# Kernel tuning notes

Hardware: AMD Instinct MI355X
Metric: run time of the kernel (lower is better)

Reference implementation:

```python
import jax, jax.numpy as jnp
import numpy as np

N_NODES = 100_000
N_EDGES = 1_600_000
N_GRAPHS = 512
IN_C, HID_C, OUT_C = 17, 64, 32


def setup_inputs() -> dict:
    key = jax.random.key(0)
    ks = jax.random.split(key, 12)
    x = jax.random.normal(ks[0], (N_NODES, IN_C), dtype=jnp.float32)
    edge_index = jax.random.randint(ks[1], (2, N_EDGES), 0, N_NODES, dtype=jnp.int64)
    batch = jnp.sort(jax.random.randint(ks[2], (N_NODES,), 0, N_GRAPHS, dtype=jnp.int64))
    def lin(k, fan_in, fan_out):
        s = 1.0 / np.sqrt(fan_in)
        kw, kb = jax.random.split(k)
        W = jax.random.uniform(kw, (fan_in, fan_out), minval=-s, maxval=s, dtype=jnp.float32)
        b = jax.random.uniform(kb, (fan_out,), minval=-s, maxval=s, dtype=jnp.float32)
        return W, b
    W1, b1 = lin(ks[3], IN_C, HID_C)      # GCNConv 1
    W2, b2 = lin(ks[4], HID_C, OUT_C)     # GCNConv 2
    Wf1, bf1 = lin(ks[5], OUT_C, OUT_C)   # fc1
    Wf2, bf2 = lin(ks[6], OUT_C, OUT_C)   # fc2
    return {"x": x, "edge_index": edge_index, "batch": batch,
            "W1": W1, "b1": b1, "W2": W2, "b2": b2,
            "Wf1": Wf1, "bf1": bf1, "Wf2": Wf2, "bf2": bf2}


def _gcn_conv(x, src, dst, norm, W, b, n_nodes):
    # PyG GCNConv: h = x @ W; out_i = sum_{j->i} norm_ij * h_j; out += bias
    h = x @ W                                   # [N, d_out]
    msg = h[src] * norm[:, None]                # gather + scale [E+N, d_out]
    out = jax.ops.segment_sum(msg, dst, num_segments=n_nodes)
    return out + b


def reference(x, edge_index, batch, W1, b1, W2, b2, Wf1, bf1, Wf2, bf2):
    n = x.shape[0]
    loops = jnp.arange(n, dtype=edge_index.dtype)
    src = jnp.concatenate([edge_index[0], loops])  # add self loops
    dst = jnp.concatenate([edge_index[1], loops])
    # symmetric normalization: deg^-1/2[src] * deg^-1/2[dst]
    deg = jax.ops.segment_sum(jnp.ones_like(dst, dtype=x.dtype), dst, num_segments=n)
    dinv = jnp.where(deg > 0, 1.0 / jnp.sqrt(deg), 0.0)
    norm = dinv[src] * dinv[dst]

    h = jax.nn.relu(_gcn_conv(x, src, dst, norm, W1, b1, n))
    h = _gcn_conv(h, src, dst, norm, W2, b2, n)

    # global mean pool over graphs
    cnt = jax.ops.segment_sum(jnp.ones((n,), dtype=h.dtype), batch, num_segments=N_GRAPHS)
    pooled = jax.ops.segment_sum(h, batch, num_segments=N_GRAPHS) / jnp.clip(cnt, 1.0)[:, None]

    out = jax.nn.relu(pooled @ Wf1 + bf1)
    out = out @ Wf2 + bf2
    return out  # [N_GRAPHS, OUT_C]
```

## Files before the change

### kernel.cpp

```cpp
#include <hip/hip_runtime.h>

#define IN_C 17
#define HID  64
#define OUTC 32

#define CH   8192
#define TA   512
#define NBP  512
#define BCAP 5632
#define SCAP 1024
#define BS_BLKS 8

typedef __attribute__((ext_vector_type(2))) float f2;
typedef __attribute__((ext_vector_type(8))) short bf16x8;
typedef __attribute__((ext_vector_type(4))) float f32x4;
__device__ __forceinline__ f2 mkf2(float x, float y) { f2 r; r.x = x; r.y = y; return r; }

__device__ __forceinline__ unsigned short f2bf(float f) {
    unsigned u = __float_as_uint(f);
    u += 0x7fffu + ((u >> 16) & 1u);
    return (unsigned short)(u >> 16);
}
__device__ __forceinline__ float bflo(unsigned u) { return __uint_as_float(u << 16); }
__device__ __forceinline__ float bfhi(unsigned u) { return __uint_as_float(u & 0xffff0000u); }

__global__ __launch_bounds__(TA) void k_binA(const int* __restrict__ src,
        const int* __restrict__ dst, int E,
        int* __restrict__ outbuf, int* __restrict__ cntmat, int* __restrict__ offmat) {
    __shared__ int cnt[NBP];
    __shared__ int off[NBP];
    __shared__ int stage[CH];
    int t = threadIdx.x;
    long base = (long)blockIdx.x * CH;
    int nE = (int)(E - base); if (nE > CH) nE = CH;
    cnt[t] = 0;
    __syncthreads();
    int bk[16], pk[16], rk[16];
#pragma unroll
    for (int j = 0; j < 16; ++j) {
        int idx = t + j * TA;
        if (idx < nE) {
            long e = base + idx;
            int d = __builtin_nontemporal_load(&dst[e]);
            int s = __builtin_nontemporal_load(&src[e]);
            int b = d >> 8;
            bk[j] = b;
            pk[j] = s | ((d & 255) << 17);
            rk[j] = atomicAdd(&cnt[b], 1);
        } else bk[j] = -1;
    }
    __syncthreads();
    int c = cnt[t];
    off[t] = c;
    __syncthreads();
    int inc = c;
    for (int s = 1; s < NBP; s <<= 1) {
        int add = (t >= s) ? off[t - s] : 0;
        __syncthreads();
        inc += add; off[t] = inc;
        __syncthreads();
    }
    int excl = inc - c;
    __syncthreads();
    off[t] = excl;
    __syncthreads();
#pragma unroll
    for (int j = 0; j < 16; ++j)
        if (bk[j] >= 0) stage[off[bk[j]] + rk[j]] = pk[j];
    __syncthreads();
    for (int i = t; i < nE; i += TA) outbuf[base + i] = stage[i];
    cntmat[blockIdx.x * NBP + t] = c;
    offmat[blockIdx.x * NBP + t] = excl;
}

__global__ __launch_bounds__(NBP) void k_bsum1(const int* __restrict__ cntmat,
        int nblkA, int* __restrict__ part, float* __restrict__ pool, int poolN) {
    int t = threadIdx.x, b = blockIdx.x;
    int per = (nblkA + BS_BLKS - 1) / BS_BLKS;
    int i0 = b * per, i1 = min(i0 + per, nblkA);
    int s = 0;
    for (int i = i0; i < i1; ++i) s += cntmat[i * NBP + t];
    part[b * NBP + t] = s;
    for (int i = b * NBP + t; i < poolN; i += BS_BLKS * NBP) pool[i] = 0.f;
}

__global__ __launch_bounds__(NBP) void k_bsum2(const int* __restrict__ part,
        int* __restrict__ bbase, const float* __restrict__ W2,
        uint4* __restrict__ w2frag) {
    __shared__ int sh[NBP];
    int t = threadIdx.x;
    int s = 0;
#pragma unroll
    for (int i = 0; i < BS_BLKS; ++i) s += part[i * NBP + t];
    sh[t] = s;
    __syncthreads();
    int inc = s;
    for (int st = 1; st < NBP; st <<= 1) {
        int add = (t >= st) ? sh[t - st] : 0;
        __syncthreads();
        inc += add; sh[t] = inc;
        __syncthreads();
    }
    bbase[t] = inc - s;
    if (t < 256) {
        int f = t >> 6, l = t & 63;
        int kt = f >> 1, nt = f & 1;
        int kbase = kt * 32 + (l >> 4) * 8;
        int c = nt * 16 + (l & 15);
        unsigned short v[8];
#pragma unroll
        for (int j = 0; j < 8; ++j) v[j] = f2bf(W2[(kbase + j) * OUTC + c]);
        uint4 o;
        o.x = (unsigned)v[0] | ((unsigned)v[1] << 16);
        o.y = (unsigned)v[2] | ((unsigned)v[3] << 16);
        o.z = (unsigned)v[4] | ((unsigned)v[5] << 16);
        o.w = (unsigned)v[6] | ((unsigned)v[7] << 16);
        w2frag[f * 64 + l] = o;
    }
}

__global__ __launch_bounds__(TA) void k_binB(const int* __restrict__ outbuf,
        const int* __restrict__ cntmat, const int* __restrict__ offmat,
        const int* __restrict__ bbase, int nblkA, int N,
        int* __restrict__ csr, int2* __restrict__ meta,
        const float* __restrict__ x, unsigned* __restrict__ xs16h,
        unsigned short* __restrict__ xs17h) {
    __shared__ int segc[256], sego[256], segs[256];
    __shared__ int ndeg[256], noff[256];
    __shared__ int stage[BCAP];
    int t = threadIdx.x, b = blockIdx.x;
    if (t < 256) {
        int cc = 0, ss = 0;
        if (t < nblkA) { cc = cntmat[t * NBP + b]; ss = offmat[t * NBP + b]; }
        segc[t] = cc; segs[t] = ss; sego[t] = cc;
        ndeg[t] = 0;
    }
    __syncthreads();
    {
        int c = (t < 256) ? sego[t] : 0;
        int inc = c;
        for (int s = 1; s < 256; s <<= 1) {
            int add = (t < 256 && t >= s) ? sego[t - s] : 0;
            __syncthreads();
            if (t < 256) { inc += add; sego[t] = inc; }
            __syncthreads();
        }
        if (t < 256) sego[t] = inc - c;
    }
    __syncthreads();
    int wave = t >> 6, lane = t & 63;
    for (int i = wave; i < nblkA; i += TA / 64) {
        int c = segc[i], so = sego[i];
        long gs = (long)i * CH + segs[i];
        for (int l = lane; l < c; l += 64) {
            int p = so + l;
            if (p < BCAP) stage[p] = __builtin_nontemporal_load(&outbuf[gs + l]);
        }
    }
    __syncthreads();
    int T = sego[255] + segc[255];
    if (T > BCAP) T = BCAP;
    int mypk[11], myrk[11], ne = 0;
    for (int k = t; k < T; k += TA) {
        int p = stage[k];
        int l = (p >> 17) & 255;
        myrk[ne] = atomicAdd(&ndeg[l], 1);
        mypk[ne] = p;
        ne++;
    }
    __syncthreads();
    {
        int c = (t < 256) ? ndeg[t] : 0;
        if (t < 256) noff[t] = c;
        __syncthreads();
        int inc = c;
        for (int s = 1; s < 256; s <<= 1) {
            int add = (t < 256 && t >= s) ? noff[t - s] : 0;
            __syncthreads();
            if (t < 256) { inc += add; noff[t] = inc; }
            __syncthreads();
        }
        if (t < 256) noff[t] = inc - c;
    }
    __syncthreads();
    int gb = bbase[b];
    int n0 = b << 8;
    if (t < 256 && n0 + t < N) {
        int n = n0 + t;
        meta[n] = make_int2(gb + noff[t], ndeg[t]);
        float dinv = rsqrtf((float)(ndeg[t] + 1));
        const float* xr = x + (size_t)n * IN_C;
        unsigned* xo = xs16h + (size_t)n * 8;
#pragma unroll
        for (int w2 = 0; w2 < 8; ++w2) {
            unsigned lo = f2bf(xr[2 * w2] * dinv);
            unsigned hi = f2bf(xr[2 * w2 + 1] * dinv);
            xo[w2] = lo | (hi << 16);
        }
        xs17h[n] = f2bf(xr[16] * dinv);
    }
    for (int j = 0; j < ne; ++j) {
        int p = mypk[j];
        int l = (p >> 17) & 255;
        csr[gb + noff[l] + myrk[j]] = p & 0x1FFFF;
    }
}

__global__ __launch_bounds__(256) void k_gather1(
        const uint4* __restrict__ xs16v, const unsigned short* __restrict__ xs17h,
        const int* __restrict__ csr, const int2* __restrict__ meta,
        const float* __restrict__ W1, const float* __restrict__ b1,
        unsigned short* __restrict__ h1b, int N) {
    __shared__ __align__(16) float aggx[16][20];
    __shared__ float dinv_sh[16];
    __shared__ int csr_sh[SCAP];

    int tid = threadIdx.x;
    int n0 = blockIdx.x * 16;
    int nlast = min(n0 + 15, N - 1);
    int2 m0 = meta[n0];
    int2 mlv = meta[nlast];
    int s_lo = m0.x;
    int seglen = mlv.x + mlv.y - s_lo;
    int sg = min(seglen, SCAP);
    for (int i = tid; i < sg; i += 256)
        csr_sh[i] = __builtin_nontemporal_load(&csr[s_lo + i]);
    int ch = tid & 63;
    float w1r[IN_C];
#pragma unroll
    for (int k = 0; k < IN_C; ++k) w1r[k] = W1[k * HID + ch];
    float b1v = b1[ch];
    __syncthreads();

    int ln = tid >> 4, sl = tid & 15;
    int n = n0 + ln;
    f2 acc[8];
#pragma unroll
    for (int j = 0; j < 8; ++j) acc[j] = mkf2(0.f, 0.f);
    float a17 = 0.f;
    if (n < N) {
        int2 m = meta[n];
        int start = m.x, cnt = m.y, end = start + cnt;
        auto body = [&](int s) {
            uint4 v0 = xs16v[(size_t)s * 2];
            uint4 v1 = xs16v[(size_t)s * 2 + 1];
            acc[0] += mkf2(bflo(v0.x), bfhi(v0.x));
            acc[1] += mkf2(bflo(v0.y), bfhi(v0.y));
            acc[2] += mkf2(bflo(v0.z), bfhi(v0.z));
            acc[3] += mkf2(bflo(v0.w), bfhi(v0.w));
            acc[4] += mkf2(bflo(v1.x), bfhi(v1.x));
            acc[5] += mkf2(bflo(v1.y), bfhi(v1.y));
            acc[6] += mkf2(bflo(v1.z), bfhi(v1.z));
            acc[7] += mkf2(bflo(v1.w), bfhi(v1.w));
            a17 += bflo((unsigned)xs17h[s]);
        };
        if (seglen <= SCAP) {
            for (int k = start + sl; k < end; k += 16) body(csr_sh[k - s_lo]);
        } else {
            for (int k = start + sl; k < end; k += 16)
                body(__builtin_nontemporal_load(&csr[k]));
        }
        if (sl == 0) {
            body(n);
            dinv_sh[ln] = rsqrtf((float)(cnt + 1));
        }
    }
    float a[16];
#pragma unroll
    for (int j = 0; j < 8; ++j) { a[2 * j] = acc[j].x; a[2 * j + 1] = acc[j].y; }
#pragma unroll
    for (int j = 0; j < 8; ++j) {
        float tt = (sl & 8) ? a[j + 8] : a[j];
        float uu = (sl & 8) ? a[j] : a[j + 8];
        a[j] = tt + __shfl_xor(uu, 8);
    }
#pragma unroll
    for (int j = 0; j < 4; ++j) {
        float tt = (sl & 4) ? a[j + 4] : a[j];
        float uu = (sl & 4) ? a[j] : a[j + 4];
        a[j] = tt + __shfl_xor(uu, 4);
    }
#pragma unroll
    for (int j = 0; j < 2; ++j) {
        float tt = (sl & 2) ? a[j + 2] : a[j];
        float uu = (sl & 2) ? a[j] : a[j + 2];
        a[j] = tt + __shfl_xor(uu, 2);
    }
    {
        float tt = (sl & 1) ? a[1] : a[0];
        float uu = (sl & 1) ? a[0] : a[1];
        a[0] = tt + __shfl_xor(uu, 1);
    }
    a17 += __shfl_xor(a17, 1);
    a17 += __shfl_xor(a17, 2);
    a17 += __shfl_xor(a17, 4);
    a17 += __shfl_xor(a17, 8);
    aggx[ln][sl] = a[0];
    if (sl == 0) aggx[ln][16] = a17;
    __syncthreads();
    int s0 = tid >> 6;
#pragma unroll
    for (int rep = 0; rep < 4; ++rep) {
        int slot = s0 + rep * 4;
        int nn = n0 + slot;
        if (nn < N) {
            const float4* ap = (const float4*)aggx[slot];
            float4 A0 = ap[0], A1 = ap[1], A2 = ap[2], A3 = ap[3];
            float a16 = aggx[slot][16];
            float dot = A0.x * w1r[0]  + A0.y * w1r[1]  + A0.z * w1r[2]  + A0.w * w1r[3]
                      + A1.x * w1r[4]  + A1.y * w1r[5]  + A1.z * w1r[6]  + A1.w * w1r[7]
                      + A2.x * w1r[8]  + A2.y * w1r[9]  + A2.z * w1r[10] + A2.w * w1r[11]
                      + A3.x * w1r[12] + A3.y * w1r[13] + A3.z * w1r[14] + A3.w * w1r[15]
                      + a16  * w1r[16];
            float dv = dinv_sh[slot];
            float r = fmaxf(dv * dot + b1v, 0.f);
            h1b[(size_t)nn * HID + ch] = f2bf(dv * r);
        }
    }
}

__global__ __launch_bounds__(256) void k_mm2f(
        const unsigned short* __restrict__ h1b, const uint4* __restrict__ w2frag,
        unsigned* __restrict__ hs2, int N) {
    int tid = threadIdx.x;
    int wv = tid >> 6, l = tid & 63;
    int n0w = blockIdx.x * 64 + wv * 16;
    int row = l & 15, kq = l >> 4;
    const bf16x8* a0p = (const bf16x8*)(h1b + (size_t)(n0w + row) * HID + kq * 8);
    const bf16x8* a1p = (const bf16x8*)(h1b + (size_t)(n0w + row) * HID + 32 + kq * 8);
    bf16x8 a0 = *a0p;
    bf16x8 a1 = *a1p;
    bf16x8 b00 = *(const bf16x8*)&w2frag[0 * 64 + l];
    bf16x8 b01 = *(const bf16x8*)&w2frag[1 * 64 + l];
    bf16x8 b10 = *(const bf16x8*)&w2frag[2 * 64 + l];
    bf16x8 b11 = *(const bf16x8*)&w2frag[3 * 64 + l];
    f32x4 d0 = {0.f, 0.f, 0.f, 0.f}, d1 = {0.f, 0.f, 0.f, 0.f};
    d0 = __builtin_amdgcn_mfma_f32_16x16x32_bf16(a0, b00, d0, 0, 0, 0);
    d0 = __builtin_amdgcn_mfma_f32_16x16x32_bf16(a1, b10, d0, 0, 0, 0);
    d1 = __builtin_amdgcn_mfma_f32_16x16x32_bf16(a0, b01, d1, 0, 0, 0);
    d1 = __builtin_amdgcn_mfma_f32_16x16x32_bf16(a1, b11, d1, 0, 0, 0);
    int wcol = l & 15;
    int rbase = (l >> 4) * 4;
#pragma unroll
    for (int r = 0; r < 4; ++r) {
        int node = n0w + rbase + r;
        if (node < N)
            hs2[(size_t)node * 16 + wcol] =
                (unsigned)f2bf(d0[r]) | ((unsigned)f2bf(d1[r]) << 16);
    }
}

__global__ __launch_bounds__(256) void k_gather2(
        const uint4* __restrict__ hs2v, const int* __restrict__ csr,
        const int2* __restrict__ meta, const float* __restrict__ b2,
        const int* __restrict__ batch, float* pool, float* cntg, int N) {
    __shared__ __align__(16) float cont[16][OUTC];
    __shared__ int bsh[16];
    __shared__ int csr_sh[SCAP];
    int tid = threadIdx.x;
    int n0 = blockIdx.x * 16;
    int nlast = min(n0 + 15, N - 1);
    int2 m0 = meta[n0];
    int2 mlv = meta[nlast];
    int s_lo = m0.x;
    int seglen = mlv.x + mlv.y - s_lo;
    int sg = min(seglen, SCAP);
    for (int i = tid; i < sg; i += 256)
        csr_sh[i] = __builtin_nontemporal_load(&csr[s_lo + i]);
    __syncthreads();

    int ln = tid >> 4, sl = tid & 15;
    int n = n0 + ln;
    f2 acc[16];
#pragma unroll
    for (int j = 0; j < 16; ++j) acc[j] = mkf2(0.f, 0.f);
    float dinv = 0.f;
    if (n < N) {
        int2 m = meta[n];
        int start = m.x, cnt = m.y, end = start + cnt;
        dinv = rsqrtf((float)(cnt + 1));
        auto body = [&](int s) {
            const uint4* rp = hs2v + (size_t)s * 4;
            uint4 v0 = rp[0], v1 = rp[1], v2 = rp[2], v3 = rp[3];
            acc[0]  += mkf2(bflo(v0.x), bfhi(v0.x));
            acc[1]  += mkf2(bflo(v0.y), bfhi(v0.y));
            acc[2]  += mkf2(bflo(v0.z), bfhi(v0.z));
            acc[3]  += mkf2(bflo(v0.w), bfhi(v0.w));
            acc[4]  += mkf2(bflo(v1.x), bfhi(v1.x));
            acc[5]  += mkf2(bflo(v1.y), bfhi(v1.y));
            acc[6]  += mkf2(bflo(v1.z), bfhi(v1.z));
            acc[7]  += mkf2(bflo(v1.w), bfhi(v1.w));
            acc[8]  += mkf2(bflo(v2.x), bfhi(v2.x));
            acc[9]  += mkf2(bflo(v2.y), bfhi(v2.y));
            acc[10] += mkf2(bflo(v2.z), bfhi(v2.z));
            acc[11] += mkf2(bflo(v2.w), bfhi(v2.w));
            acc[12] += mkf2(bflo(v3.x), bfhi(v3.x));
            acc[13] += mkf2(bflo(v3.y), bfhi(v3.y));
            acc[14] += mkf2(bflo(v3.z), bfhi(v3.z));
            acc[15] += mkf2(bflo(v3.w), bfhi(v3.w));
        };
        if (seglen <= SCAP) {
            for (int k = start + sl; k < end; k += 16) body(csr_sh[k - s_lo]);
        } else {
            for (int k = start + sl; k < end; k += 16)
                body(__builtin_nontemporal_load(&csr[k]));
        }
        if (sl == 0) body(n);
    }
    float a[32];
#pragma unroll
    for (int j = 0; j < 16; ++j) { a[2 * j] = acc[j].x; a[2 * j + 1] = acc[j].y; }
#pragma unroll
    for (int j = 0; j < 16; ++j) {
        float tt = (sl & 8) ? a[j + 16] : a[j];
        float uu = (sl & 8) ? a[j] : a[j + 16];
        a[j] = tt + __shfl_xor(uu, 8);
    }
#pragma unroll
    for (int j = 0; j < 8; ++j) {
        float tt = (sl & 4) ? a[j + 8] : a[j];
        float uu = (sl & 4) ? a[j] : a[j + 8];
        a[j] = tt + __shfl_xor(uu, 4);
    }
#pragma unroll
    for (int j = 0; j < 4; ++j) {
        float tt = (sl & 2) ? a[j + 4] : a[j];
        float uu = (sl & 2) ? a[j] : a[j + 4];
        a[j] = tt + __shfl_xor(uu, 2);
    }
#pragma unroll
    for (int j = 0; j < 2; ++j) {
        float tt = (sl & 1) ? a[j + 2] : a[j];
        float uu = (sl & 1) ? a[j] : a[j + 2];
        a[j] = tt + __shfl_xor(uu, 1);
    }
    if (n < N) {
        cont[ln][sl]      = dinv * a[0] + b2[sl];
        cont[ln][sl + 16] = dinv * a[1] + b2[sl + 16];
        if (sl == 0) bsh[ln] = batch[n];
    } else {
        cont[ln][sl] = 0.f;
        cont[ln][sl + 16] = 0.f;
        if (sl == 0) bsh[ln] = -1;
    }
    __syncthreads();
    if (tid < OUTC) {
        int c = tid;
        float run = 0.f; int cur = -1;
        for (int j = 0; j < 16; ++j) {
            int bj = bsh[j];
            if (bj < 0) continue;
            if (bj == cur) run += cont[j][c];
            else {
                if (cur >= 0) atomicAdd(&pool[(size_t)cur * OUTC + c], run);
                cur = bj; run = cont[j][c];
            }
        }
        if (cur >= 0) atomicAdd(&pool[(size_t)cur * OUTC + c], run);
        if (c == 0) {
            float crun = 0.f; cur = -1;
            for (int j = 0; j < 16; ++j) {
                int bj = bsh[j];
                if (bj < 0) continue;
                if (bj == cur) crun += 1.f;
                else {
                    if (cur >= 0) atomicAdd(&cntg[cur], crun);
                    cur = bj; crun = 1.f;
                }
            }
            if (cur >= 0) atomicAdd(&cntg[cur], crun);
        }
    }
}

__global__ void k_final(const float* __restrict__ pool, const float* __restrict__ cntg,
                        const float* __restrict__ Wf1, const float* __restrict__ bf1,
                        const float* __restrict__ Wf2, const float* __restrict__ bf2,
                        float* out, int G) {
    __shared__ float p[OUTC], t[OUTC];
    int g = blockIdx.x;
    int c = threadIdx.x;
    float csafe = fmaxf(cntg[g], 1.0f);
    p[c] = pool[g * OUTC + c] / csafe;
    __syncthreads();
    float acc = bf1[c];
#pragma unroll
    for (int k = 0; k < OUTC; ++k) acc += p[k] * Wf1[k * OUTC + c];
    t[c] = fmaxf(acc, 0.f);
    __syncthreads();
    float acc2 = bf2[c];
#pragma unroll
    for (int k = 0; k < OUTC; ++k) acc2 += t[k] * Wf2[k * OUTC + c];
    out[g * OUTC + c] = acc2;
}

extern "C" void kernel_launch(void* const* d_in, const int* in_sizes, int n_in,
                              void* d_out, int out_size, void* d_ws, size_t ws_size,
                              hipStream_t stream) {
    const float* x    = (const float*)d_in[0];
    const int*   ei   = (const int*)  d_in[1];
    const int*   batch= (const int*)  d_in[2];
    const float* W1   = (const float*)d_in[3];
    const float* b1   = (const float*)d_in[4];
    const float* W2   = (const float*)d_in[5];
    const float* b2   = (const float*)d_in[6];
    const float* Wf1  = (const float*)d_in[7];
    const float* bf1  = (const float*)d_in[8];
    const float* Wf2  = (const float*)d_in[9];
    const float* bf2  = (const float*)d_in[10];

    const int N = in_sizes[0] / IN_C;
    const int E = in_sizes[1] / 2;
    const int G = out_size / OUTC;
    const int* src = ei;
    const int* dst = ei + E;

    const int nblkA = (E + CH - 1) / CH;
    const int NB    = (N + 255) >> 8;

    char* w = (char*)d_ws;
    int*   csr      = (int*)w;   w += (size_t)E * sizeof(int);
    int2*  meta     = (int2*)w;  w += (size_t)N * sizeof(int2);
    unsigned* xs16h = (unsigned*)w; w += (size_t)N * 8 * sizeof(unsigned);
    unsigned* hs2   = (unsigned*)w; w += (size_t)N * 16 * sizeof(unsigned);
    unsigned short* xs17h = (unsigned short*)w; w += (size_t)N * sizeof(unsigned short);
    w = (char*)(((size_t)w + 15) & ~(size_t)15);
    float* pool     = (float*)w; w += (size_t)G * OUTC * sizeof(float);
    float* cntg     = (float*)w; w += (size_t)G * sizeof(float);
    w = (char*)(((size_t)w + 15) & ~(size_t)15);
    int*   outbuf   = (int*)w;   w += (size_t)E * sizeof(int);
    int*   cntmat   = (int*)w;   w += (size_t)nblkA * NBP * sizeof(int);
    int*   offmat   = (int*)w;   w += (size_t)nblkA * NBP * sizeof(int);
    int*   bbase    = (int*)w;   w += NBP * sizeof(int);
    int*   part     = (int*)w;   w += BS_BLKS * NBP * sizeof(int);
    w = (char*)(((size_t)w + 15) & ~(size_t)15);
    unsigned short* h1b = (unsigned short*)w; w += (size_t)(N + 64) * HID * sizeof(unsigned short);
    uint4* w2frag   = (uint4*)w; w += 4 * 64 * sizeof(uint4);

    const int poolN = G * OUTC + G;

    k_binA<<<nblkA, TA, 0, stream>>>(src, dst, E, outbuf, cntmat, offmat);
    k_bsum1<<<BS_BLKS, NBP, 0, stream>>>(cntmat, nblkA, part, pool, poolN);
    k_bsum2<<<1, NBP, 0, stream>>>(part, bbase, W2, w2frag);
    k_binB<<<NB, TA, 0, stream>>>(outbuf, cntmat, offmat, bbase, nblkA, N,
                                  csr, meta, x, xs16h, xs17h);

    dim3 blk(256);
    k_gather1<<<(N + 15) / 16, blk, 0, stream>>>((const uint4*)xs16h, xs17h, csr, meta,
                                                 W1, b1, h1b, N);

    k_mm2f<<<(N + 63) / 64, blk, 0, stream>>>(h1b, w2frag, hs2, N);

    k_gather2<<<(N + 15) / 16, blk, 0, stream>>>((const uint4*)hs2, csr, meta,
                                                 b2, batch, pool, cntg, N);

    k_final<<<G, OUTC, 0, stream>>>(pool, cntg, Wf1, bf1, Wf2, bf2, (float*)d_out, G);
}
```

Baseline: 130.7 us.

## Fuse second-layer MFMA projection into first gather kernel via shared memory

The layer-1 activations are now kept in shared memory inside the first gather kernel, and two waves immediately run the bf16 MFMA against W2 fragments, writing hs2 directly. This removes the separate k_mm2f launch and the global write and read of the N x 64 bf16 h1 buffer. The hs2 layout changes from interleaved column pairs to a plain 32-column bf16 row, so gather2's bias indexing and contribution stores are adjusted to match. The cost is extra shared memory per block, a further barrier, and only half the waves doing the MFMA tail.

```diff
diff --git a/kernel.cpp b/kernel.cpp
--- a/kernel.cpp
+++ b/kernel.cpp
@@ -210,9 +210,10 @@
         const uint4* __restrict__ xs16v, const unsigned short* __restrict__ xs17h,
         const int* __restrict__ csr, const int2* __restrict__ meta,
         const float* __restrict__ W1, const float* __restrict__ b1,
-        unsigned short* __restrict__ h1b, int N) {
+        const uint4* __restrict__ w2frag, unsigned short* __restrict__ hs2u, int N) {
     __shared__ __align__(16) float aggx[16][20];
     __shared__ float dinv_sh[16];
+    __shared__ __align__(16) float h1sh[16][68];
     __shared__ int csr_sh[SCAP];
 
     int tid = threadIdx.x;
@@ -313,40 +314,38 @@
                       + A3.x * w1r[12] + A3.y * w1r[13] + A3.z * w1r[14] + A3.w * w1r[15]
                       + a16  * w1r[16];
             float dv = dinv_sh[slot];
-            float r = fmaxf(dv * dot + b1v, 0.f);
-            h1b[(size_t)nn * HID + ch] = f2bf(dv * r);
-        }
-    }
-}
-
-__global__ __launch_bounds__(256) void k_mm2f(
-        const unsigned short* __restrict__ h1b, const uint4* __restrict__ w2frag,
-        unsigned* __restrict__ hs2, int N) {
-    int tid = threadIdx.x;
+            h1sh[slot][ch] = dv * fmaxf(dv * dot + b1v, 0.f);
+        }
+    }
+    __syncthreads();
     int wv = tid >> 6, l = tid & 63;
-    int n0w = blockIdx.x * 64 + wv * 16;
-    int row = l & 15, kq = l >> 4;
-    const bf16x8* a0p = (const bf16x8*)(h1b + (size_t)(n0w + row) * HID + kq * 8);
-    const bf16x8* a1p = (const bf16x8*)(h1b + (size_t)(n0w + row) * HID + 32 + kq * 8);
-    bf16x8 a0 = *a0p;
-    bf16x8 a1 = *a1p;
-    bf16x8 b00 = *(const bf16x8*)&w2frag[0 * 64 + l];
-    bf16x8 b01 = *(const bf16x8*)&w2frag[1 * 64 + l];
-    bf16x8 b10 = *(const bf16x8*)&w2frag[2 * 64 + l];
-    bf16x8 b11 = *(const bf16x8*)&w2frag[3 * 64 + l];
-    f32x4 d0 = {0.f, 0.f, 0.f, 0.f}, d1 = {0.f, 0.f, 0.f, 0.f};
-    d0 = __builtin_amdgcn_mfma_f32_16x16x32_bf16(a0, b00, d0, 0, 0, 0);
-    d0 = __builtin_amdgcn_mfma_f32_16x16x32_bf16(a1, b10, d0, 0, 0, 0);
-    d1 = __builtin_amdgcn_mfma_f32_16x16x32_bf16(a0, b01, d1, 0, 0, 0);
-    d1 = __builtin_amdgcn_mfma_f32_16x16x32_bf16(a1, b11, d1, 0, 0, 0);
-    int wcol = l & 15;
-    int rbase = (l >> 4) * 4;
-#pragma unroll
-    for (int r = 0; r < 4; ++r) {
-        int node = n0w + rbase + r;
-        if (node < N)
-            hs2[(size_t)node * 16 + wcol] =
-                (unsigned)f2bf(d0[r]) | ((unsigned)f2bf(d1[r]) << 16);
+    if (wv < 2) {
+        int row = l & 15, kq = l >> 4;
+        const float4* hp = (const float4*)&h1sh[row][kq * 8];
+        float4 f0v = hp[0], f1v = hp[1];
+        const float4* hq = (const float4*)&h1sh[row][32 + kq * 8];
+        float4 g0v = hq[0], g1v = hq[1];
+        bf16x8 a0, a1;
+        a0[0] = (short)f2bf(f0v.x); a0[1] = (short)f2bf(f0v.y);
+        a0[2] = (short)f2bf(f0v.z); a0[3] = (short)f2bf(f0v.w);
+        a0[4] = (short)f2bf(f1v.x); a0[5] = (short)f2bf(f1v.y);
+        a0[6] = (short)f2bf(f1v.z); a0[7] = (short)f2bf(f1v.w);
+        a1[0] = (short)f2bf(g0v.x); a1[1] = (short)f2bf(g0v.y);
+        a1[2] = (short)f2bf(g0v.z); a1[3] = (short)f2bf(g0v.w);
+        a1[4] = (short)f2bf(g1v.x); a1[5] = (short)f2bf(g1v.y);
+        a1[6] = (short)f2bf(g1v.z); a1[7] = (short)f2bf(g1v.w);
+        bf16x8 bA = *(const bf16x8*)&w2frag[(0 + wv) * 64 + l];
+        bf16x8 bB = *(const bf16x8*)&w2frag[(2 + wv) * 64 + l];
+        f32x4 d = {0.f, 0.f, 0.f, 0.f};
+        d = __builtin_amdgcn_mfma_f32_16x16x32_bf16(a0, bA, d, 0, 0, 0);
+        d = __builtin_amdgcn_mfma_f32_16x16x32_bf16(a1, bB, d, 0, 0, 0);
+        int rbase = (l >> 4) * 4;
+#pragma unroll
+        for (int r = 0; r < 4; ++r) {
+            int node = n0 + rbase + r;
+            if (node < N)
+                hs2u[(size_t)node * 32 + wv * 16 + (l & 15)] = f2bf(d[r]);
+        }
     }
 }
 
@@ -435,12 +434,12 @@
         a[j] = tt + __shfl_xor(uu, 1);
     }
     if (n < N) {
-        cont[ln][sl]      = dinv * a[0] + b2[sl];
-        cont[ln][sl + 16] = dinv * a[1] + b2[sl + 16];
+        float c0 = dinv * a[0] + b2[2 * sl];
+        float c1 = dinv * a[1] + b2[2 * sl + 1];
+        *(float2*)&cont[ln][2 * sl] = make_float2(c0, c1);
         if (sl == 0) bsh[ln] = batch[n];
     } else {
-        cont[ln][sl] = 0.f;
-        cont[ln][sl + 16] = 0.f;
+        *(float2*)&cont[ln][2 * sl] = make_float2(0.f, 0.f);
         if (sl == 0) bsh[ln] = -1;
     }
     __syncthreads();
@@ -534,7 +533,6 @@
     int*   bbase    = (int*)w;   w += NBP * sizeof(int);
     int*   part     = (int*)w;   w += BS_BLKS * NBP * sizeof(int);
     w = (char*)(((size_t)w + 15) & ~(size_t)15);
-    unsigned short* h1b = (unsigned short*)w; w += (size_t)(N + 64) * HID * sizeof(unsigned short);
     uint4* w2frag   = (uint4*)w; w += 4 * 64 * sizeof(uint4);
 
     const int poolN = G * OUTC + G;
@@ -547,9 +545,8 @@
 
     dim3 blk(256);
     k_gather1<<<(N + 15) / 16, blk, 0, stream>>>((const uint4*)xs16h, xs17h, csr, meta,
-                                                 W1, b1, h1b, N);
-
-    k_mm2f<<<(N + 63) / 64, blk, 0, stream>>>(h1b, w2frag, hs2, N);
+                                                 W1, b1, w2frag,
+                                                 (unsigned short*)hs2, N);
 
     k_gather2<<<(N + 15) / 16, blk, 0, stream>>>((const uint4*)hs2, csr, meta,
                                                  b2, batch, pool, cntg, N);
```

Result: faster. 125.3 us (-4.1%).
